# Optimization experiments

Hardware: AMD Instinct MI355X
Metric: run time of the kernel (lower is better)

## Reference

```python
import jax, jax.numpy as jnp
import numpy as np

N = 2_000_000  # number of poses
EPS_THETA = 1e-6  # small-angle threshold from original module


def setup_inputs() -> dict:
    key = jax.random.key(0)
    k1, k2 = jax.random.split(key)
    xi = jax.random.normal(k1, (N, 6), dtype=jnp.float32) * 0.1  # (n,6) lie-algebra params
    poses_init = jax.random.normal(k2, (N, 4, 4), dtype=jnp.float32)  # (n,4,4) initial poses
    return {"xi": xi, "poses_init": poses_init}


def _skew(v):
    # v: (n,3) -> (n,3,3) skew-symmetric matrices
    z = jnp.zeros_like(v[..., 0])
    return jnp.stack([
        jnp.stack([z, -v[..., 2], v[..., 1]], axis=-1),
        jnp.stack([v[..., 2], z, -v[..., 0]], axis=-1),
        jnp.stack([-v[..., 1], v[..., 0], z], axis=-1),
    ], axis=-2)


def reference(xi, poses_init):
    # xi: (n,6) = [translation t (3), rotation omega (3)]
    t = xi[:, :3]
    omega = xi[:, 3:]
    theta = jnp.linalg.norm(omega, axis=-1)            # (n,)
    small = theta < EPS_THETA
    safe_theta = jnp.where(small, jnp.ones_like(theta), theta)
    k = omega / safe_theta[:, None]                    # unit axis
    K = _skew(k)                                       # (n,3,3)
    I3 = jnp.eye(3, dtype=xi.dtype)
    s = jnp.sin(theta)[:, None, None]
    c = (1.0 - jnp.cos(theta))[:, None, None]
    R_rod = I3 + s * K + c * jnp.einsum('nij,njk->nik', K, K)
    R_small = I3 + _skew(omega)                        # first-order branch as in original
    R = jnp.where(small[:, None, None], R_small, R_rod)  # (n,3,3)

    # assemble (n,4,4) homogeneous transform [[R, t], [0, 1]]
    top = jnp.concatenate([R, t[:, :, None]], axis=-1)               # (n,3,4)
    bottom_row = jnp.array([0.0, 0.0, 0.0, 1.0], dtype=xi.dtype)
    bottom = jnp.broadcast_to(bottom_row, (xi.shape[0], 1, 4))
    T = jnp.concatenate([top, bottom], axis=1)                       # (n,4,4)

    # right-multiply by initial poses: delta @ pose_init
    return jnp.einsum('nij,njk->nik', T, poses_init)
```

## Files before the change

### kernel.cpp

```cpp
#include <hip/hip_runtime.h>

typedef float fx4 __attribute__((ext_vector_type(4)));

__device__ __forceinline__ void nt_store4(float4* p, float4 v) {
    fx4 vv = {v.x, v.y, v.z, v.w};
    __builtin_nontemporal_store(vv, (fx4*)p);
}

template<int CTRL>
__device__ __forceinline__ float qperm(float v) {
    return __int_as_float(__builtin_amdgcn_update_dpp(
        0, __float_as_int(v), CTRL, 0xF, 0xF, true));
}
template<int CTRL>
__device__ __forceinline__ float4 qperm4(float4 v) {
    float4 r;
    r.x = qperm<CTRL>(v.x);
    r.y = qperm<CTRL>(v.y);
    r.z = qperm<CTRL>(v.z);
    r.w = qperm<CTRL>(v.w);
    return r;
}

#define ROT1 0xC9
#define ROT2 0xD2
#define BC3  0xFF

__global__ __launch_bounds__(256) void se3_compose_kernel(
    const float* __restrict__ xi,
    const float4* __restrict__ poses4,
    float4* __restrict__ out4,
    int n4)
{
    int i = blockIdx.x * blockDim.x + threadIdx.x;
    if (i >= n4) return;

    int p = i >> 2;
    int r = i & 3;

    const float2* x2 = (const float2*)(xi + 6ll * p);
    float2 a  = x2[0];
    float2 b  = x2[1];
    float2 cc = x2[2];
    float t0 = a.x, t1 = a.y, t2 = b.x;
    float w0 = b.y, w1 = cc.x, w2 = cc.y;

    float4 pr = poses4[i];

    float x = w0 * w0 + w1 * w1 + w2 * w2;
    float A, B;
    if (__builtin_expect(x < 2.25f, 1)) {
        A = 1.0f + x * (-1.0f / 6.0f  + x * (1.0f / 120.0f + x * (-1.0f / 5040.0f  + x * (1.0f / 362880.0f))));
        B = 0.5f + x * (-1.0f / 24.0f + x * (1.0f / 720.0f + x * (-1.0f / 40320.0f + x * (1.0f / 3628800.0f))));
    } else {
        float th = sqrtf(x);
        A = sinf(th) / th;
        B = (1.0f - cosf(th)) / x;
    }

    float wr = (r == 0) ? w0 : (r == 1) ? w1 : w2;
    float tr = (r == 0) ? t0 : (r == 1) ? t1 : (r == 2) ? t2 : 0.0f;

    float wa = qperm<ROT1>(wr);
    float wb = qperm<ROT2>(wr);

    float4 Pa = qperm4<ROT1>(pr);
    float4 Pb = qperm4<ROT2>(pr);
    float4 P3 = qperm4<BC3>(pr);

    float diag = 1.0f - B * (wa * wa + wb * wb);
    float off1 = B * wr * wa - A * wb;
    float off2 = B * wr * wb + A * wa;
    if (r == 3) { diag = 1.0f; off1 = 0.0f; off2 = 0.0f; }

    float4 o;
    o.x = diag * pr.x + off1 * Pa.x + off2 * Pb.x + tr * P3.x;
    o.y = diag * pr.y + off1 * Pa.y + off2 * Pb.y + tr * P3.y;
    o.z = diag * pr.z + off1 * Pa.z + off2 * Pb.z + tr * P3.z;
    o.w = diag * pr.w + off1 * Pa.w + off2 * Pb.w + tr * P3.w;

    nt_store4(&out4[i], o);
}

extern "C" void kernel_launch(void* const* d_in, const int* in_sizes, int n_in,
                              void* d_out, int out_size, void* d_ws, size_t ws_size,
                              hipStream_t stream) {
    const float*  xi     = (const float*)d_in[0];
    const float4* poses4 = (const float4*)d_in[1];
    float4*       out4   = (float4*)d_out;

    int n  = in_sizes[0] / 6;
    int n4 = 4 * n;

    const int block = 256;
    const int grid  = (n4 + block - 1) / block;
    se3_compose_kernel<<<grid, block, 0, stream>>>(xi, poses4, out4, n4);
}
```

Before: 249.1 us.

## Process two poses per thread and load xi once per lane with DPP broadcast

Each thread now handles two rows drawn from two halves of the pose array, which halves the grid and doubles the independent loads in flight per thread. Instead of every lane reading all six xi floats, each lane loads one float2 and the values are broadcast across the quad with DPP. This targets redundant xi load traffic and raises memory-level parallelism. It relies on n being even so the halves split cleanly; with an odd n the second half would be misindexed.

```diff
diff --git a/kernel.cpp b/kernel.cpp
--- a/kernel.cpp
+++ b/kernel.cpp
@@ -24,28 +24,17 @@
 
 #define ROT1 0xC9
 #define ROT2 0xD2
+#define BC0  0x00
+#define BC1  0x55
+#define BC2  0xAA
 #define BC3  0xFF
 
-__global__ __launch_bounds__(256) void se3_compose_kernel(
-    const float* __restrict__ xi,
-    const float4* __restrict__ poses4,
-    float4* __restrict__ out4,
-    int n4)
+__device__ __forceinline__ float4 compose_row(
+    float2 f0, float2 f1, float2 f2_,
+    float4 pr, int r)
 {
-    int i = blockIdx.x * blockDim.x + threadIdx.x;
-    if (i >= n4) return;
-
-    int p = i >> 2;
-    int r = i & 3;
-
-    const float2* x2 = (const float2*)(xi + 6ll * p);
-    float2 a  = x2[0];
-    float2 b  = x2[1];
-    float2 cc = x2[2];
-    float t0 = a.x, t1 = a.y, t2 = b.x;
-    float w0 = b.y, w1 = cc.x, w2 = cc.y;
-
-    float4 pr = poses4[i];
+    float t0 = f0.x, t1 = f0.y, t2 = f1.x;
+    float w0 = f1.y, w1 = f2_.x, w2 = f2_.y;
 
     float x = w0 * w0 + w1 * w1 + w2 * w2;
     float A, B;
@@ -78,8 +67,43 @@
     o.y = diag * pr.y + off1 * Pa.y + off2 * Pb.y + tr * P3.y;
     o.z = diag * pr.z + off1 * Pa.z + off2 * Pb.z + tr * P3.z;
     o.w = diag * pr.w + off1 * Pa.w + off2 * Pb.w + tr * P3.w;
+    return o;
+}
 
-    nt_store4(&out4[i], o);
+__global__ __launch_bounds__(256) void se3_compose_kernel(
+    const float* __restrict__ xi,
+    const float4* __restrict__ poses4,
+    float4* __restrict__ out4,
+    int n2)
+{
+    int i = blockIdx.x * blockDim.x + threadIdx.x;
+    if (i >= n2) return;
+
+    int r = i & 3;
+    long long p0 = (long long)(i >> 2);
+    long long p1 = p0 + (n2 >> 2);
+
+    int rc = (r < 2) ? r : 2;
+    const float2* xA = (const float2*)(xi + 6ll * p0);
+    const float2* xB = (const float2*)(xi + 6ll * p1);
+    float2 fa = xA[rc];
+    float2 fb = xB[rc];
+
+    float4 pr0 = poses4[i];
+    float4 pr1 = poses4[i + n2];
+
+    float2 a0; a0.x = qperm<BC0>(fa.x); a0.y = qperm<BC0>(fa.y);
+    float2 a1; a1.x = qperm<BC1>(fa.x); a1.y = qperm<BC1>(fa.y);
+    float2 a2; a2.x = qperm<BC2>(fa.x); a2.y = qperm<BC2>(fa.y);
+    float2 b0; b0.x = qperm<BC0>(fb.x); b0.y = qperm<BC0>(fb.y);
+    float2 b1; b1.x = qperm<BC1>(fb.x); b1.y = qperm<BC1>(fb.y);
+    float2 b2; b2.x = qperm<BC2>(fb.x); b2.y = qperm<BC2>(fb.y);
+
+    float4 o0 = compose_row(a0, a1, a2, pr0, r);
+    float4 o1 = compose_row(b0, b1, b2, pr1, r);
+
+    nt_store4(&out4[i],      o0);
+    nt_store4(&out4[i + n2], o1);
 }
 
 extern "C" void kernel_launch(void* const* d_in, const int* in_sizes, int n_in,
@@ -90,9 +114,9 @@
     float4*       out4   = (float4*)d_out;
 
     int n  = in_sizes[0] / 6;
-    int n4 = 4 * n;
+    int n2 = 2 * n;
 
     const int block = 256;
-    const int grid  = (n4 + block - 1) / block;
-    se3_compose_kernel<<<grid, block, 0, stream>>>(xi, poses4, out4, n4);
+    const int grid  = (n2 + block - 1) / block;
+    se3_compose_kernel<<<grid, block, 0, stream>>>(xi, poses4, out4, n2);
 }
```

Measured after the change: 252.2 us. About the same (+1.3%).

## Use grid-stride persistent loop with software-prefetched next iteration loads

Applied to the files above, without the earlier changes.

Replaces the one-thread-per-row launch with a grid capped at 2048 blocks and a grid-stride loop. Each thread issues the pose and xi loads for its next row before computing and storing the current one, so load latency overlaps with compute. The stride is a multiple of 4, so each thread keeps the same row index inside its quad and the DPP quad permutes stay valid. The cost is that far fewer threads are resident to hide memory latency, in a kernel that is bound by memory bandwidth.

```diff
diff --git a/kernel.cpp b/kernel.cpp
--- a/kernel.cpp
+++ b/kernel.cpp
@@ -26,26 +26,12 @@
 #define ROT2 0xD2
 #define BC3  0xFF
 
-__global__ __launch_bounds__(256) void se3_compose_kernel(
-    const float* __restrict__ xi,
-    const float4* __restrict__ poses4,
-    float4* __restrict__ out4,
-    int n4)
+__device__ __forceinline__ float4 compose_row(
+    float2 f0, float2 f1, float2 f2_,
+    float4 pr, int r)
 {
-    int i = blockIdx.x * blockDim.x + threadIdx.x;
-    if (i >= n4) return;
-
-    int p = i >> 2;
-    int r = i & 3;
-
-    const float2* x2 = (const float2*)(xi + 6ll * p);
-    float2 a  = x2[0];
-    float2 b  = x2[1];
-    float2 cc = x2[2];
-    float t0 = a.x, t1 = a.y, t2 = b.x;
-    float w0 = b.y, w1 = cc.x, w2 = cc.y;
-
-    float4 pr = poses4[i];
+    float t0 = f0.x, t1 = f0.y, t2 = f1.x;
+    float w0 = f1.y, w1 = f2_.x, w2 = f2_.y;
 
     float x = w0 * w0 + w1 * w1 + w2 * w2;
     float A, B;
@@ -78,7 +64,40 @@
     o.y = diag * pr.y + off1 * Pa.y + off2 * Pb.y + tr * P3.y;
     o.z = diag * pr.z + off1 * Pa.z + off2 * Pb.z + tr * P3.z;
     o.w = diag * pr.w + off1 * Pa.w + off2 * Pb.w + tr * P3.w;
+    return o;
+}
 
+__global__ __launch_bounds__(256) void se3_compose_kernel(
+    const float* __restrict__ xi,
+    const float4* __restrict__ poses4,
+    float4* __restrict__ out4,
+    int n4)
+{
+    int tid    = blockIdx.x * blockDim.x + threadIdx.x;
+    int stride = gridDim.x * blockDim.x;
+    if (tid >= n4) return;
+
+    int r = tid & 3;
+
+    int i = tid;
+    float4 pr = poses4[i];
+    const float2* x2 = (const float2*)(xi + 6ll * (i >> 2));
+    float2 f0 = x2[0], f1 = x2[1], f2_ = x2[2];
+
+    int inext = i + stride;
+    while (inext < n4) {
+        float4 prN = poses4[inext];
+        const float2* x2N = (const float2*)(xi + 6ll * (inext >> 2));
+        float2 f0N = x2N[0], f1N = x2N[1], f2N = x2N[2];
+
+        float4 o = compose_row(f0, f1, f2_, pr, r);
+        nt_store4(&out4[i], o);
+
+        i = inext; inext += stride;
+        pr = prN; f0 = f0N; f1 = f1N; f2_ = f2N;
+    }
+
+    float4 o = compose_row(f0, f1, f2_, pr, r);
     nt_store4(&out4[i], o);
 }
 
@@ -93,6 +112,7 @@
     int n4 = 4 * n;
 
     const int block = 256;
-    const int grid  = (n4 + block - 1) / block;
+    int grid = (n4 + block - 1) / block;
+    if (grid > 2048) grid = 2048;
     se3_compose_kernel<<<grid, block, 0, stream>>>(xi, poses4, out4, n4);
 }
```

Result: slower. 254.8 us (+2.3%).
